# Kernel optimization log

Measured on AMD Instinct MI355X. Metric: run time of the kernel, lower is better.

Reference implementation:

```python
import jax, jax.numpy as jnp
import numpy as np

EPS = 0.3
LAYERS = 2


def setup_inputs() -> dict:
    key = jax.random.key(0)
    ks = jax.random.split(key, 8)
    N, F, H, C, E = 50000, 512, 128, 40, 800000

    def xavier(k, shape):
        fan_out, fan_in = shape[0], shape[-1]
        std = 1.414 * np.sqrt(2.0 / (fan_in + fan_out))
        return (jax.random.normal(k, shape, jnp.float32) * std).astype(jnp.float32)

    return {
        "x": jax.random.normal(ks[0], (N, F), jnp.float32),
        "t1_w": xavier(ks[1], (H, F)),
        "t1_b": jnp.zeros((H,), jnp.float32),
        "t2_w": xavier(ks[2], (C, H)),
        "t2_b": jnp.zeros((C,), jnp.float32),
        "gate_w": xavier(ks[3], (LAYERS, 2 * H)),  # Linear(2H,1) weight per layer
        "gate_b": jnp.zeros((LAYERS,), jnp.float32),
        "edge_index": jax.random.randint(ks[4], (2, E), 0, N, jnp.int32),
    }


def reference(x, t1_w, t1_b, t2_w, t2_b, gate_w, gate_b, edge_index):
    N = x.shape[0]
    H = t1_w.shape[0]
    row, col = edge_index[0], edge_index[1]  # source, target

    # norm_degree = degree(row).clamp(min=1) ** -0.5
    deg = jax.ops.segment_sum(jnp.ones_like(row, dtype=x.dtype), row, num_segments=N)
    nd = jnp.clip(deg, 1.0) ** -0.5  # [N]
    nd_r, nd_c = nd[row], nd[col]    # [E]

    # dropout is identity in eval mode
    h = jax.nn.relu(x @ t1_w.T + t1_b)  # [N,H]
    raw = h
    for l in range(LAYERS):
        h_src = h[row]  # x_j, [E,H]
        h_dst = h[col]  # [E,H]
        # gate(cat([h[row], h[col]])) == h_src @ W[:H] + h_dst @ W[H:] + b
        g = jnp.tanh(h_src @ gate_w[l, :H] + h_dst @ gate_w[l, H:] + gate_b[l])  # [E]
        norm = g * nd_r * nd_c  # [E]
        agg = jax.ops.segment_sum(norm[:, None] * h_src, col, num_segments=N)  # scatter-add at targets
        h = EPS * raw + agg
    out = h @ t2_w.T + t2_b  # [N,C]
    return jax.nn.log_softmax(out, axis=1)
```

## Files before the change

kernel.cpp:

```cpp
#include <hip/hip_runtime.h>
#include <math.h>

#define F_DIM 512
#define H_DIM 128
#define C_DIM 40
#define EPS_F 0.3f
#define NBLK 256

typedef float f32x4 __attribute__((ext_vector_type(4)));
typedef unsigned int u32x4 __attribute__((ext_vector_type(4)));
typedef __bf16 bf16x8 __attribute__((ext_vector_type(8)));
typedef unsigned short ushort_t;
typedef unsigned char uchar_t;

__device__ inline float bflo(unsigned t) { return __builtin_bit_cast(float, t << 16); }
__device__ inline float bfhi(unsigned t) { return __builtin_bit_cast(float, t & 0xffff0000u); }
__device__ inline unsigned short f2bf(float f) {
  unsigned u = __builtin_bit_cast(unsigned, f);
  u = (u + 0x7fffu + ((u >> 16) & 1u)) >> 16;
  return (unsigned short)u;
}
__device__ inline unsigned pack2bf(float a, float b) {
  unsigned ua = __builtin_bit_cast(unsigned, a);
  unsigned ub = __builtin_bit_cast(unsigned, b);
  ua = (ua + 0x7fffu + ((ua >> 16) & 1u)) >> 16;
  ub = (ub + 0x7fffu + ((ub >> 16) & 1u)) >> 16;
  return ua | (ub << 16);
}


__global__ __launch_bounds__(256) void part_count(const int* __restrict__ row,
    const int* __restrict__ col, int* __restrict__ blkhist, int E, int nbkt, int chunk) {
  __shared__ int ch[256], rh[256];
  int t = threadIdx.x, b = blockIdx.x;
  ch[t] = 0; rh[t] = 0;
  __syncthreads();
  int s = b * chunk, e = min(E, s + chunk);
  for (int i = s + t; i < e; i += 256) {
    atomicAdd(&ch[((unsigned)col[i]) >> 8], 1);
    atomicAdd(&rh[((unsigned)row[i]) >> 8], 1);
  }
  __syncthreads();
  if (t < nbkt) {
    blkhist[t * NBLK + b] = ch[t];
    blkhist[(nbkt + t) * NBLK + b] = rh[t];
  }
}

__global__ __launch_bounds__(256) void part_scatter(const int* __restrict__ row,
    const int* __restrict__ col, const int* __restrict__ blkhist,
    int* __restrict__ bktbase, unsigned* __restrict__ colpart,
    uchar_t* __restrict__ rowpart, int E, int nbkt, int chunk) {
  __shared__ int sbase[400];
  __shared__ int stot[400];
  __shared__ int psum[256];
  __shared__ int sc[400];
  __shared__ int coff[400];
  int t = threadIdx.x, b = blockIdx.x;
  int nrows = 2 * nbkt;
  for (int rr = t; rr < nrows; rr += 256) {
    const int* rp = &blkhist[rr * NBLK];
    int pre = 0, tot = 0;
    for (int i = 0; i < NBLK; ++i) {
      int v = rp[i];
      pre += (i < b) ? v : 0;
      tot += v;
    }
    sbase[rr] = pre; stot[rr] = tot;
  }
  __syncthreads();
  int e0 = (2 * t     < nrows) ? stot[2 * t]     : 0;
  int e1 = (2 * t + 1 < nrows) ? stot[2 * t + 1] : 0;
  psum[t] = e0 + e1;
  __syncthreads();
  for (int off = 1; off < 256; off <<= 1) {
    int add = (t >= off) ? psum[t - off] : 0;
    __syncthreads();
    psum[t] += add;
    __syncthreads();
  }
  int pex = (t == 0) ? 0 : psum[t - 1];
  if (2 * t < nrows)     sc[2 * t]     = pex + sbase[2 * t];
  if (2 * t + 1 < nrows) sc[2 * t + 1] = pex + e0 + sbase[2 * t + 1];
  if (b == 0) {
    if (2 * t < nrows)     bktbase[2 * t]     = pex;
    if (2 * t + 1 < nrows) bktbase[2 * t + 1] = pex + e0;
    if (t == 0) bktbase[nrows] = 2 * E;
  }
  for (int rr = t; rr < nrows; rr += 256) coff[rr] = 0;
  __syncthreads();
  int s = b * chunk, e = min(E, s + chunk);
  for (int i = s + t; i < e; i += 256) {
    unsigned c = (unsigned)col[i], r = (unsigned)row[i];
    int bc = (int)(c >> 8), br = (int)(r >> 8);
    int pc = sc[bc] + atomicAdd(&coff[bc], 1);
    colpart[pc] = (r << 8) | (c & 255u);
    int pr = sc[nbkt + br] + atomicAdd(&coff[nbkt + br], 1) - E;
    rowpart[pr] = (uchar_t)(r & 255u);
  }
}

__global__ __launch_bounds__(256) void bucket_both(const unsigned* __restrict__ colpart,
    const uchar_t* __restrict__ rowpart, const int* __restrict__ bktbase,
    int* __restrict__ col_ptr, int* __restrict__ csr_src, float* __restrict__ nd,
    int N, int E, int nbkt) {
  __shared__ int cnt[256], ex[256], off[256];
  int t = threadIdx.x, bb = blockIdx.x;
  if (bb < nbkt) {
    int bkt = bb;
    int s = bktbase[bkt], e = bktbase[bkt + 1];
    cnt[t] = 0; off[t] = 0;
    __syncthreads();
    for (int i = s + t; i < e; i += 256)
      atomicAdd(&cnt[(int)(colpart[i] & 255u)], 1);
    __syncthreads();
    ex[t] = cnt[t];
    __syncthreads();
    for (int o = 1; o < 256; o <<= 1) {
      int v = (t >= o) ? ex[t - o] : 0;
      __syncthreads();
      ex[t] += v;
      __syncthreads();
    }
    int excl = (t == 0) ? 0 : ex[t - 1];
    __syncthreads();
    ex[t] = excl;
    __syncthreads();
    int node = bkt * 256 + t;
    if (node < N) col_ptr[node] = s + ex[t];
    if (bkt == 0 && t == 0) col_ptr[N] = E;
    for (int i = s + t; i < e; i += 256) {
      unsigned p = colpart[i];
      int lb = (int)(p & 255u);
      int dst = s + ex[lb] + atomicAdd(&off[lb], 1);
      csr_src[dst] = (int)(p >> 8);
    }
  } else {
    int bkt = bb - nbkt;
    int s = bktbase[nbkt + bkt] - E, e = bktbase[nbkt + bkt + 1] - E;
    cnt[t] = 0;
    __syncthreads();
    for (int i = s + t; i < e; i += 256)
      atomicAdd(&cnt[(int)rowpart[i]], 1);
    __syncthreads();
    int node = bkt * 256 + t;
    if (node < N) {
      int d = cnt[t] < 1 ? 1 : cnt[t];
      nd[node] = 1.0f / sqrtf((float)d);
    }
  }
}


__global__ __launch_bounds__(256) void gemm1_mfma(const float* __restrict__ x,
    const float* __restrict__ w, const float* __restrict__ b,
    const float* __restrict__ gwl, const float* __restrict__ gb,
    const float* __restrict__ nd,
    ushort_t* __restrict__ hbf, float2* __restrict__ pack0,
    float* __restrict__ s2a, int N) {
  __shared__ u32x4 AsBuf[1024];
  __shared__ u32x4 BsBuf[1024];
  char* Asc = (char*)AsBuf;
  char* Bsc = (char*)BsBuf;

  int t = threadIdx.x;
  int lane = t & 63;
  int wid = t >> 6;
  int wm = wid >> 1;
  int wn = wid & 1;
  int m0 = blockIdx.x * 128;
  int ql = lane & 15;

  f32x4 acc[4][4];
#pragma unroll
  for (int i = 0; i < 4; ++i)
#pragma unroll
    for (int j = 0; j < 4; ++j) acc[i][j] = (f32x4){0.f, 0.f, 0.f, 0.f};

  float bias[4], g1v[4], g2v[4];
#pragma unroll
  for (int j = 0; j < 4; ++j) {
    int c = wn * 64 + j * 16 + ql;
    bias[j] = b[c];
    g1v[j] = gwl[c];
    g2v[j] = gwl[H_DIM + c];
  }

  for (int kk = 0; kk < F_DIM; kk += 64) {
#pragma unroll
    for (int q = 0; q < 4; ++q) {
      int c = q * 256 + t;
      int row = c >> 3, kc = c & 7;
      int gm = m0 + row;
      f32x4 v0 = {0.f, 0.f, 0.f, 0.f}, v1 = {0.f, 0.f, 0.f, 0.f};
      if (gm < N) {
        const float* src = &x[(size_t)gm * F_DIM + kk + kc * 8];
        v0 = *(const f32x4*)src;
        v1 = *(const f32x4*)(src + 4);
      }
      u32x4 pk;
      pk[0] = pack2bf(v0[0], v0[1]);
      pk[1] = pack2bf(v0[2], v0[3]);
      pk[2] = pack2bf(v1[0], v1[1]);
      pk[3] = pack2bf(v1[2], v1[3]);
      *(u32x4*)(Asc + row * 128 + ((kc ^ (row & 7)) << 4)) = pk;
    }
#pragma unroll
    for (int q = 0; q < 4; ++q) {
      int c = q * 256 + t;
      int row = c >> 3, kc = c & 7;
      const float* src = &w[(size_t)row * F_DIM + kk + kc * 8];
      f32x4 v0 = *(const f32x4*)src;
      f32x4 v1 = *(const f32x4*)(src + 4);
      u32x4 pk;
      pk[0] = pack2bf(v0[0], v0[1]);
      pk[1] = pack2bf(v0[2], v0[3]);
      pk[2] = pack2bf(v1[0], v1[1]);
      pk[3] = pack2bf(v1[2], v1[3]);
      *(u32x4*)(Bsc + row * 128 + ((kc ^ (row & 7)) << 4)) = pk;
    }
    __syncthreads();
#pragma unroll
    for (int kh = 0; kh < 2; ++kh) {
      bf16x8 af[4], bfr[4];
      int kc = kh * 4 + (lane >> 4);
#pragma unroll
      for (int i = 0; i < 4; ++i) {
        int row = wm * 64 + i * 16 + ql;
        af[i] = *(const bf16x8*)(Asc + row * 128 + ((kc ^ (row & 7)) << 4));
      }
#pragma unroll
      for (int j = 0; j < 4; ++j) {
        int row = wn * 64 + j * 16 + ql;
        bfr[j] = *(const bf16x8*)(Bsc + row * 128 + ((kc ^ (row & 7)) << 4));
      }
#pragma unroll
      for (int i = 0; i < 4; ++i)
#pragma unroll
        for (int j = 0; j < 4; ++j)
          acc[i][j] = __builtin_amdgcn_mfma_f32_16x16x32_bf16(af[i], bfr[j], acc[i][j], 0, 0, 0);
    }
    __syncthreads();
  }

  float gp1[4][4], gp2[4][4];
#pragma unroll
  for (int i = 0; i < 4; ++i)
#pragma unroll
    for (int r = 0; r < 4; ++r) { gp1[i][r] = 0.f; gp2[i][r] = 0.f; }

#pragma unroll
  for (int i = 0; i < 4; ++i) {
    int rbase = m0 + wm * 64 + i * 16 + ((lane >> 4) * 4);
#pragma unroll
    for (int j = 0; j < 4; ++j) {
      int col = wn * 64 + j * 16 + ql;
#pragma unroll
      for (int r = 0; r < 4; ++r) {
        int gr = rbase + r;
        float o = fmaxf(acc[i][j][r] + bias[j], 0.f);
        if (gr < N) hbf[(size_t)gr * H_DIM + col] = f2bf(o);
        gp1[i][r] = fmaf(o, g1v[j], gp1[i][r]);
        gp2[i][r] = fmaf(o, g2v[j], gp2[i][r]);
      }
    }
  }
#pragma unroll
  for (int i = 0; i < 4; ++i)
#pragma unroll
    for (int r = 0; r < 4; ++r) {
#pragma unroll
      for (int m = 1; m < 16; m <<= 1) {
        gp1[i][r] += __shfl_xor(gp1[i][r], m);
        gp2[i][r] += __shfl_xor(gp2[i][r], m);
      }
    }
  float* pgA = (float*)AsBuf;
  float* pgB = (float*)AsBuf + 256;
  if (ql == 0) {
#pragma unroll
    for (int i = 0; i < 4; ++i)
#pragma unroll
      for (int r = 0; r < 4; ++r) {
        int lr = wm * 64 + i * 16 + (lane >> 4) * 4 + r;
        pgA[lr * 2 + wn] = gp1[i][r];
        pgB[lr * 2 + wn] = gp2[i][r];
      }
  }
  __syncthreads();
  if (t < 128) {
    int gr = m0 + t;
    if (gr < N) {
      float p1 = pgA[t * 2] + pgA[t * 2 + 1];
      float p2 = pgB[t * 2] + pgB[t * 2 + 1];
      float ndv = nd[gr];
      pack0[gr] = make_float2(p1, ndv);
      s2a[gr] = p2 + gb[0];
    }
  }
}


template <int MODE>
__global__ __launch_bounds__(256) void agg_kernel(const ushort_t* __restrict__ hbf,
    const ushort_t* __restrict__ rawbf, const float2* __restrict__ pack,
    const float* __restrict__ s2pb, const float* __restrict__ nd,
    const int* __restrict__ col_ptr, const int* __restrict__ csr_src,
    ushort_t* __restrict__ houtbf,
    const float* __restrict__ gwl, const float* __restrict__ gb,
    float2* __restrict__ packo, float* __restrict__ s2o,
    const float* __restrict__ w2, const float* __restrict__ b2,
    float* __restrict__ out, int N) {
  __shared__ float ws[(MODE == 2 ? C_DIM : 1)][129];
  __shared__ float bsh[(MODE == 2 ? C_DIM : 1)];
  __shared__ float hsm[(MODE == 2 ? 4 : 1)][H_DIM];
  int t = threadIdx.x;
  int wave = t >> 6, lane = t & 63;
  int g = lane >> 4, q = lane & 15;
  if (MODE == 2) {
    for (int i = t; i < C_DIM * H_DIM; i += 256) ws[i / H_DIM][i % H_DIM] = w2[i];
    if (t < C_DIM) bsh[t] = b2[t];
    __syncthreads();
  }
  int v = blockIdx.x * 4 + wave;
  bool act = v < N;

  float acc8[8];
#pragma unroll
  for (int k = 0; k < 8; ++k) acc8[k] = 0.f;
  float o[8];
  float ndv = 0.f;

  if (act) {
    int p0 = col_ptr[v], p1 = col_ptr[v + 1];
    float s2v = s2pb[v];
    ndv = nd[v];
    for (int base = p0; base < p1; base += 64) {
      int idx = base + lane;
      int u = 0;
      float cf = 0.f;
      if (idx < p1) {
        u = csr_src[idx];
        float2 pk = pack[u];
        cf = tanhf(pk.x + s2v) * pk.y * ndv;
      }
      int cnt = p1 - base;
      if (cnt > 64) cnt = 64;
      for (int j = 0; j < cnt; j += 4) {
        int e = j + g;
        int ue = __shfl(u, e);
        float ce = __shfl(cf, e);
        u32x4 hv = *(const u32x4*)&hbf[(size_t)ue * H_DIM + q * 8];
        acc8[0] = fmaf(ce, bflo(hv[0]), acc8[0]);
        acc8[1] = fmaf(ce, bfhi(hv[0]), acc8[1]);
        acc8[2] = fmaf(ce, bflo(hv[1]), acc8[2]);
        acc8[3] = fmaf(ce, bfhi(hv[1]), acc8[3]);
        acc8[4] = fmaf(ce, bflo(hv[2]), acc8[4]);
        acc8[5] = fmaf(ce, bfhi(hv[2]), acc8[5]);
        acc8[6] = fmaf(ce, bflo(hv[3]), acc8[6]);
        acc8[7] = fmaf(ce, bfhi(hv[3]), acc8[7]);
      }
    }
#pragma unroll
    for (int k = 0; k < 8; ++k) {
      acc8[k] += __shfl_xor(acc8[k], 16);
      acc8[k] += __shfl_xor(acc8[k], 32);
    }
    u32x4 rv = *(const u32x4*)&rawbf[(size_t)v * H_DIM + q * 8];
    o[0] = fmaf(EPS_F, bflo(rv[0]), acc8[0]);
    o[1] = fmaf(EPS_F, bfhi(rv[0]), acc8[1]);
    o[2] = fmaf(EPS_F, bflo(rv[1]), acc8[2]);
    o[3] = fmaf(EPS_F, bfhi(rv[1]), acc8[3]);
    o[4] = fmaf(EPS_F, bflo(rv[2]), acc8[4]);
    o[5] = fmaf(EPS_F, bfhi(rv[2]), acc8[5]);
    o[6] = fmaf(EPS_F, bflo(rv[3]), acc8[6]);
    o[7] = fmaf(EPS_F, bfhi(rv[3]), acc8[7]);

    if (MODE == 1) {
      if (g == 0) {
        u32x4 pk;
        pk[0] = pack2bf(o[0], o[1]);
        pk[1] = pack2bf(o[2], o[3]);
        pk[2] = pack2bf(o[4], o[5]);
        pk[3] = pack2bf(o[6], o[7]);
        *(u32x4*)&houtbf[(size_t)v * H_DIM + q * 8] = pk;
      }
      f32x4 ga0 = *(const f32x4*)&gwl[q * 8];
      f32x4 ga1 = *(const f32x4*)&gwl[q * 8 + 4];
      f32x4 gb0 = *(const f32x4*)&gwl[H_DIM + q * 8];
      f32x4 gb1 = *(const f32x4*)&gwl[H_DIM + q * 8 + 4];
      float q1 = o[0] * ga0[0] + o[1] * ga0[1] + o[2] * ga0[2] + o[3] * ga0[3]
               + o[4] * ga1[0] + o[5] * ga1[1] + o[6] * ga1[2] + o[7] * ga1[3];
      float q2 = o[0] * gb0[0] + o[1] * gb0[1] + o[2] * gb0[2] + o[3] * gb0[3]
               + o[4] * gb1[0] + o[5] * gb1[1] + o[6] * gb1[2] + o[7] * gb1[3];
#pragma unroll
      for (int m = 1; m < 16; m <<= 1) {
        q1 += __shfl_xor(q1, m);
        q2 += __shfl_xor(q2, m);
      }
      if (lane == 0) {
        packo[v] = make_float2(q1, ndv);
        s2o[v] = q2 + gb[0];
      }
    }
  }

  if (MODE == 2) {
    if (act && g == 0) {
#pragma unroll
      for (int k = 0; k < 8; ++k) hsm[wave][q * 8 + k] = o[k];
    }
    __syncthreads();
    float accv = 0.f;
    if (act && lane < C_DIM) {
#pragma unroll 8
      for (int k = 0; k < H_DIM; ++k)
        accv = fmaf(hsm[wave][k], ws[lane][k], accv);
      accv += bsh[lane];
    }
    float m = (lane < C_DIM) ? accv : -1e30f;
    for (int off = 32; off > 0; off >>= 1) m = fmaxf(m, __shfl_xor(m, off));
    float ex = (lane < C_DIM) ? expf(accv - m) : 0.f;
    float s = ex;
    for (int off = 32; off > 0; off >>= 1) s += __shfl_xor(s, off);
    float lse = m + logf(s);
    if (act && lane < C_DIM) out[(size_t)v * C_DIM + lane] = accv - lse;
  }
}


extern "C" void kernel_launch(void* const* d_in, const int* in_sizes, int n_in,
                              void* d_out, int out_size, void* d_ws, size_t ws_size,
                              hipStream_t stream) {
  const float* x   = (const float*)d_in[0];
  const float* t1w = (const float*)d_in[1];
  const float* t1b = (const float*)d_in[2];
  const float* t2w = (const float*)d_in[3];
  const float* t2b = (const float*)d_in[4];
  const float* gw  = (const float*)d_in[5];
  const float* gb  = (const float*)d_in[6];
  const int*   ei  = (const int*)d_in[7];
  const int N = in_sizes[0] / F_DIM;
  const int E = in_sizes[7] / 2;
  float* out = (float*)d_out;

  char* p = (char*)d_ws;
  auto take = [&](size_t bytes) {
    char* r = p;
    p += (bytes + 255) & ~(size_t)255;
    return r;
  };
  ushort_t* h0 = (ushort_t*)take((size_t)N * H_DIM * 2);
  ushort_t* h1 = (ushort_t*)take((size_t)N * H_DIM * 2);
  float2* pack0 = (float2*)take((size_t)N * 8);
  float2* pack1 = (float2*)take((size_t)N * 8);
  float* s2a = (float*)take((size_t)N * 4);
  float* s2b = (float*)take((size_t)N * 4);
  float* nd  = (float*)take((size_t)N * 4);
  int* col_ptr = (int*)take((size_t)(N + 1) * 4);
  int* csr_src = (int*)take((size_t)E * 4);

  const int nbkt = (N + 255) >> 8;
  const int chunk = (E + NBLK - 1) / NBLK;

  int* blkhist = (int*)take((size_t)2 * nbkt * NBLK * 4);
  int* bktbase = (int*)take((size_t)(2 * nbkt + 1) * 4);
  unsigned* colpart = (unsigned*)take((size_t)E * 4);
  uchar_t* rowpart  = (uchar_t*)take((size_t)E);

  const int* row = ei;
  const int* col = ei + E;

  part_count<<<NBLK, 256, 0, stream>>>(row, col, blkhist, E, nbkt, chunk);
  part_scatter<<<NBLK, 256, 0, stream>>>(row, col, blkhist, bktbase, colpart, rowpart, E, nbkt, chunk);
  bucket_both<<<2 * nbkt, 256, 0, stream>>>(colpart, rowpart, bktbase, col_ptr, csr_src, nd, N, E, nbkt);

  gemm1_mfma<<<(N + 127) / 128, 256, 0, stream>>>(x, t1w, t1b, gw, gb, nd, h0, pack0, s2a, N);

  int nwb = (N + 3) / 4;
  agg_kernel<1><<<nwb, 256, 0, stream>>>(h0, h0, pack0, s2a, nd, col_ptr, csr_src, h1,
                                         gw + 2 * H_DIM, gb + 1, pack1, s2b,
                                         nullptr, nullptr, nullptr, N);
  agg_kernel<2><<<nwb, 256, 0, stream>>>(h1, h0, pack1, s2b, nd, col_ptr, csr_src, nullptr,
                                         nullptr, nullptr, nullptr, nullptr,
                                         t2w, t2b, out, N);
}
```

Before: 192.6 us.

## Restructure aggregation to one-edge-per-wave with 2 features per lane and unrolled gathers

```diff
diff --git a/kernel.cpp b/kernel.cpp
--- a/kernel.cpp
+++ b/kernel.cpp
@@ -26,6 +26,10 @@
   ua = (ua + 0x7fffu + ((ua >> 16) & 1u)) >> 16;
   ub = (ub + 0x7fffu + ((ub >> 16) & 1u)) >> 16;
   return ua | (ub << 16);
+}
+__device__ inline float fast_tanh(float x) {
+  float e = __expf(2.0f * x);
+  return 1.0f - 2.0f / (e + 1.0f);
 }
 
 
@@ -301,131 +305,146 @@
 }
 
 
-template <int MODE>
-__global__ __launch_bounds__(256) void agg_kernel(const ushort_t* __restrict__ hbf,
+#define AGG_CORE(HSRC)                                                          \
+  float ax = 0.f, ay = 0.f;                                                     \
+  {                                                                             \
+    int p0 = col_ptr[v], p1v = col_ptr[v + 1];                                  \
+    float s2v = s2pb[v];                                                        \
+    for (int base = p0; base < p1v; base += 64) {                               \
+      int idx = base + lane;                                                    \
+      int u = 0;                                                                \
+      float cf = 0.f;                                                           \
+      if (idx < p1v) {                                                          \
+        u = csr_src[idx];                                                       \
+        float2 pk = pack[u];                                                    \
+        cf = fast_tanh(pk.x + s2v) * pk.y * ndv;                                \
+      }                                                                         \
+      int cnt = p1v - base;                                                     \
+      if (cnt > 64) cnt = 64;                                                   \
+      int j = 0;                                                                \
+      for (; j + 8 <= cnt; j += 8) {                                            \
+        int u0 = __shfl(u, j + 0), u1 = __shfl(u, j + 1);                       \
+        int u2 = __shfl(u, j + 2), u3 = __shfl(u, j + 3);                       \
+        int u4 = __shfl(u, j + 4), u5 = __shfl(u, j + 5);                       \
+        int u6 = __shfl(u, j + 6), u7 = __shfl(u, j + 7);                       \
+        unsigned t0 = *(const unsigned*)&HSRC[(size_t)u0 * H_DIM + lane * 2];   \
+        unsigned t1 = *(const unsigned*)&HSRC[(size_t)u1 * H_DIM + lane * 2];   \
+        unsigned t2 = *(const unsigned*)&HSRC[(size_t)u2 * H_DIM + lane * 2];   \
+        unsigned t3 = *(const unsigned*)&HSRC[(size_t)u3 * H_DIM + lane * 2];   \
+        unsigned t4 = *(const unsigned*)&HSRC[(size_t)u4 * H_DIM + lane * 2];   \
+        unsigned t5 = *(const unsigned*)&HSRC[(size_t)u5 * H_DIM + lane * 2];   \
+        unsigned t6 = *(const unsigned*)&HSRC[(size_t)u6 * H_DIM + lane * 2];   \
+        unsigned t7 = *(const unsigned*)&HSRC[(size_t)u7 * H_DIM + lane * 2];   \
+        float c0 = __shfl(cf, j + 0), c1 = __shfl(cf, j + 1);                   \
+        float c2 = __shfl(cf, j + 2), c3 = __shfl(cf, j + 3);                   \
+        float c4 = __shfl(cf, j + 4), c5 = __shfl(cf, j + 5);                   \
+        float c6 = __shfl(cf, j + 6), c7 = __shfl(cf, j + 7);                   \
+        ax = fmaf(c0, bflo(t0), ax); ay = fmaf(c0, bfhi(t0), ay);               \
+        ax = fmaf(c1, bflo(t1), ax); ay = fmaf(c1, bfhi(t1), ay);               \
+        ax = fmaf(c2, bflo(t2), ax); ay = fmaf(c2, bfhi(t2), ay);               \
+        ax = fmaf(c3, bflo(t3), ax); ay = fmaf(c3, bfhi(t3), ay);               \
+        ax = fmaf(c4, bflo(t4), ax); ay = fmaf(c4, bfhi(t4), ay);               \
+        ax = fmaf(c5, bflo(t5), ax); ay = fmaf(c5, bfhi(t5), ay);               \
+        ax = fmaf(c6, bflo(t6), ax); ay = fmaf(c6, bfhi(t6), ay);               \
+        ax = fmaf(c7, bflo(t7), ax); ay = fmaf(c7, bfhi(t7), ay);               \
+      }                                                                         \
+      for (; j + 4 <= cnt; j += 4) {                                            \
+        int u0 = __shfl(u, j + 0), u1 = __shfl(u, j + 1);                       \
+        int u2 = __shfl(u, j + 2), u3 = __shfl(u, j + 3);                       \
+        unsigned t0 = *(const unsigned*)&HSRC[(size_t)u0 * H_DIM + lane * 2];   \
+        unsigned t1 = *(const unsigned*)&HSRC[(size_t)u1 * H_DIM + lane * 2];   \
+        unsigned t2 = *(const unsigned*)&HSRC[(size_t)u2 * H_DIM + lane * 2];   \
+        unsigned t3 = *(const unsigned*)&HSRC[(size_t)u3 * H_DIM + lane * 2];   \
+        float c0 = __shfl(cf, j + 0), c1 = __shfl(cf, j + 1);                   \
+        float c2 = __shfl(cf, j + 2), c3 = __shfl(cf, j + 3);                   \
+        ax = fmaf(c0, bflo(t0), ax); ay = fmaf(c0, bfhi(t0), ay);               \
+        ax = fmaf(c1, bflo(t1), ax); ay = fmaf(c1, bfhi(t1), ay);               \
+        ax = fmaf(c2, bflo(t2), ax); ay = fmaf(c2, bfhi(t2), ay);               \
+        ax = fmaf(c3, bflo(t3), ax); ay = fmaf(c3, bfhi(t3), ay);               \
+      }                                                                         \
+      for (; j < cnt; ++j) {                                                    \
+        int uj = __shfl(u, j);                                                  \
+        float cj = __shfl(cf, j);                                               \
+        unsigned tj = *(const unsigned*)&HSRC[(size_t)uj * H_DIM + lane * 2];   \
+        ax = fmaf(cj, bflo(tj), ax); ay = fmaf(cj, bfhi(tj), ay);               \
+      }                                                                         \
+    }                                                                           \
+  }
+
+__global__ __launch_bounds__(256) void agg1(const ushort_t* __restrict__ hbf,
+    const float2* __restrict__ pack, const float* __restrict__ s2pb,
+    const float* __restrict__ nd, const int* __restrict__ col_ptr,
+    const int* __restrict__ csr_src, ushort_t* __restrict__ houtbf,
+    const float* __restrict__ gwl, const float* __restrict__ gb1,
+    float2* __restrict__ packo, float* __restrict__ s2o, int N) {
+  int t = threadIdx.x;
+  int v = blockIdx.x * 4 + (t >> 6);
+  int lane = t & 63;
+  if (v >= N) return;
+  float ndv = nd[v];
+  unsigned rv = *(const unsigned*)&hbf[(size_t)v * H_DIM + lane * 2];
+  AGG_CORE(hbf)
+  float ox = fmaf(EPS_F, bflo(rv), ax);
+  float oy = fmaf(EPS_F, bfhi(rv), ay);
+  *(unsigned*)&houtbf[(size_t)v * H_DIM + lane * 2] = pack2bf(ox, oy);
+  float2 g1 = *(const float2*)&gwl[lane * 2];
+  float2 g2 = *(const float2*)&gwl[H_DIM + lane * 2];
+  float q1 = ox * g1.x + oy * g1.y;
+  float q2 = ox * g2.x + oy * g2.y;
+#pragma unroll
+  for (int off = 32; off > 0; off >>= 1) {
+    q1 += __shfl_xor(q1, off);
+    q2 += __shfl_xor(q2, off);
+  }
+  if (lane == 0) {
+    packo[v] = make_float2(q1, ndv);
+    s2o[v] = q2 + gb1[0];
+  }
+}
+
+__global__ __launch_bounds__(256) void agg2(const ushort_t* __restrict__ hbf,
     const ushort_t* __restrict__ rawbf, const float2* __restrict__ pack,
     const float* __restrict__ s2pb, const float* __restrict__ nd,
     const int* __restrict__ col_ptr, const int* __restrict__ csr_src,
-    ushort_t* __restrict__ houtbf,
-    const float* __restrict__ gwl, const float* __restrict__ gb,
-    float2* __restrict__ packo, float* __restrict__ s2o,
     const float* __restrict__ w2, const float* __restrict__ b2,
     float* __restrict__ out, int N) {
-  __shared__ float ws[(MODE == 2 ? C_DIM : 1)][129];
-  __shared__ float bsh[(MODE == 2 ? C_DIM : 1)];
-  __shared__ float hsm[(MODE == 2 ? 4 : 1)][H_DIM];
+  __shared__ float ws[C_DIM][129];
+  __shared__ float bsh[C_DIM];
+  __shared__ float hsm[4][H_DIM];
   int t = threadIdx.x;
+  for (int i = t; i < C_DIM * H_DIM; i += 256) ws[i / H_DIM][i % H_DIM] = w2[i];
+  if (t < C_DIM) bsh[t] = b2[t];
+  __syncthreads();
   int wave = t >> 6, lane = t & 63;
-  int g = lane >> 4, q = lane & 15;
-  if (MODE == 2) {
-    for (int i = t; i < C_DIM * H_DIM; i += 256) ws[i / H_DIM][i % H_DIM] = w2[i];
-    if (t < C_DIM) bsh[t] = b2[t];
-    __syncthreads();
-  }
   int v = blockIdx.x * 4 + wave;
   bool act = v < N;
-
-  float acc8[8];
-#pragma unroll
-  for (int k = 0; k < 8; ++k) acc8[k] = 0.f;
-  float o[8];
-  float ndv = 0.f;
-
+  float ox = 0.f, oy = 0.f;
   if (act) {
-    int p0 = col_ptr[v], p1 = col_ptr[v + 1];
-    float s2v = s2pb[v];
-    ndv = nd[v];
-    for (int base = p0; base < p1; base += 64) {
-      int idx = base + lane;
-      int u = 0;
-      float cf = 0.f;
-      if (idx < p1) {
-        u = csr_src[idx];
-        float2 pk = pack[u];
-        cf = tanhf(pk.x + s2v) * pk.y * ndv;
-      }
-      int cnt = p1 - base;
-      if (cnt > 64) cnt = 64;
-      for (int j = 0; j < cnt; j += 4) {
-        int e = j + g;
-        int ue = __shfl(u, e);
-        float ce = __shfl(cf, e);
-        u32x4 hv = *(const u32x4*)&hbf[(size_t)ue * H_DIM + q * 8];
-        acc8[0] = fmaf(ce, bflo(hv[0]), acc8[0]);
-        acc8[1] = fmaf(ce, bfhi(hv[0]), acc8[1]);
-        acc8[2] = fmaf(ce, bflo(hv[1]), acc8[2]);
-        acc8[3] = fmaf(ce, bfhi(hv[1]), acc8[3]);
-        acc8[4] = fmaf(ce, bflo(hv[2]), acc8[4]);
-        acc8[5] = fmaf(ce, bfhi(hv[2]), acc8[5]);
-        acc8[6] = fmaf(ce, bflo(hv[3]), acc8[6]);
-        acc8[7] = fmaf(ce, bfhi(hv[3]), acc8[7]);
-      }
-    }
-#pragma unroll
-    for (int k = 0; k < 8; ++k) {
-      acc8[k] += __shfl_xor(acc8[k], 16);
-      acc8[k] += __shfl_xor(acc8[k], 32);
-    }
-    u32x4 rv = *(const u32x4*)&rawbf[(size_t)v * H_DIM + q * 8];
-    o[0] = fmaf(EPS_F, bflo(rv[0]), acc8[0]);
-    o[1] = fmaf(EPS_F, bfhi(rv[0]), acc8[1]);
-    o[2] = fmaf(EPS_F, bflo(rv[1]), acc8[2]);
-    o[3] = fmaf(EPS_F, bfhi(rv[1]), acc8[3]);
-    o[4] = fmaf(EPS_F, bflo(rv[2]), acc8[4]);
-    o[5] = fmaf(EPS_F, bfhi(rv[2]), acc8[5]);
-    o[6] = fmaf(EPS_F, bflo(rv[3]), acc8[6]);
-    o[7] = fmaf(EPS_F, bfhi(rv[3]), acc8[7]);
-
-    if (MODE == 1) {
-      if (g == 0) {
-        u32x4 pk;
-        pk[0] = pack2bf(o[0], o[1]);
-        pk[1] = pack2bf(o[2], o[3]);
-        pk[2] = pack2bf(o[4], o[5]);
-        pk[3] = pack2bf(o[6], o[7]);
-        *(u32x4*)&houtbf[(size_t)v * H_DIM + q * 8] = pk;
-      }
-      f32x4 ga0 = *(const f32x4*)&gwl[q * 8];
-      f32x4 ga1 = *(const f32x4*)&gwl[q * 8 + 4];
-      f32x4 gb0 = *(const f32x4*)&gwl[H_DIM + q * 8];
-      f32x4 gb1 = *(const f32x4*)&gwl[H_DIM + q * 8 + 4];
-      float q1 = o[0] * ga0[0] + o[1] * ga0[1] + o[2] * ga0[2] + o[3] * ga0[3]
-               + o[4] * ga1[0] + o[5] * ga1[1] + o[6] * ga1[2] + o[7] * ga1[3];
-      float q2 = o[0] * gb0[0] + o[1] * gb0[1] + o[2] * gb0[2] + o[3] * gb0[3]
-               + o[4] * gb1[0] + o[5] * gb1[1] + o[6] * gb1[2] + o[7] * gb1[3];
-#pragma unroll
-      for (int m = 1; m < 16; m <<= 1) {
-        q1 += __shfl_xor(q1, m);
-        q2 += __shfl_xor(q2, m);
-      }
-      if (lane == 0) {
-        packo[v] = make_float2(q1, ndv);
-        s2o[v] = q2 + gb[0];
-      }
-    }
-  }
-
-  if (MODE == 2) {
-    if (act && g == 0) {
-#pragma unroll
-      for (int k = 0; k < 8; ++k) hsm[wave][q * 8 + k] = o[k];
-    }
-    __syncthreads();
-    float accv = 0.f;
-    if (act && lane < C_DIM) {
+    float ndv = nd[v];
+    unsigned rv = *(const unsigned*)&rawbf[(size_t)v * H_DIM + lane * 2];
+    AGG_CORE(hbf)
+    ox = fmaf(EPS_F, bflo(rv), ax);
+    oy = fmaf(EPS_F, bfhi(rv), ay);
+    hsm[wave][lane * 2] = ox;
+    hsm[wave][lane * 2 + 1] = oy;
+  }
+  __syncthreads();
+  float accv = 0.f;
+  if (act && lane < C_DIM) {
 #pragma unroll 8
-      for (int k = 0; k < H_DIM; ++k)
-        accv = fmaf(hsm[wave][k], ws[lane][k], accv);
-      accv += bsh[lane];
-    }
-    float m = (lane < C_DIM) ? accv : -1e30f;
-    for (int off = 32; off > 0; off >>= 1) m = fmaxf(m, __shfl_xor(m, off));
-    float ex = (lane < C_DIM) ? expf(accv - m) : 0.f;
-    float s = ex;
-    for (int off = 32; off > 0; off >>= 1) s += __shfl_xor(s, off);
-    float lse = m + logf(s);
-    if (act && lane < C_DIM) out[(size_t)v * C_DIM + lane] = accv - lse;
-  }
+    for (int k = 0; k < H_DIM; ++k)
+      accv = fmaf(hsm[wave][k], ws[lane][k], accv);
+    accv += bsh[lane];
+  }
+  float m = (lane < C_DIM) ? accv : -1e30f;
+#pragma unroll
+  for (int off = 32; off > 0; off >>= 1) m = fmaxf(m, __shfl_xor(m, off));
+  float ex = (lane < C_DIM) ? expf(accv - m) : 0.f;
+  float s = ex;
+#pragma unroll
+  for (int off = 32; off > 0; off >>= 1) s += __shfl_xor(s, off);
+  float lse = m + logf(s);
+  if (act && lane < C_DIM) out[(size_t)v * C_DIM + lane] = accv - lse;
 }
 
 
@@ -478,10 +497,8 @@
   gemm1_mfma<<<(N + 127) / 128, 256, 0, stream>>>(x, t1w, t1b, gw, gb, nd, h0, pack0, s2a, N);
 
   int nwb = (N + 3) / 4;
-  agg_kernel<1><<<nwb, 256, 0, stream>>>(h0, h0, pack0, s2a, nd, col_ptr, csr_src, h1,
-                                         gw + 2 * H_DIM, gb + 1, pack1, s2b,
-                                         nullptr, nullptr, nullptr, N);
-  agg_kernel<2><<<nwb, 256, 0, stream>>>(h1, h0, pack1, s2b, nd, col_ptr, csr_src, nullptr,
-                                         nullptr, nullptr, nullptr, nullptr,
-                                         t2w, t2b, out, N);
-}
+  agg1<<<nwb, 256, 0, stream>>>(h0, pack0, s2a, nd, col_ptr, csr_src, h1,
+                                gw + 2 * H_DIM, gb + 1, pack1, s2b, N);
+  agg2<<<nwb, 256, 0, stream>>>(h1, h0, pack1, s2b, nd, col_ptr, csr_src,
+                                t2w, t2b, out, N);
+}
```

Result: faster. 187.2 us (-2.8%).
